# Optimization experiments

Hardware: AMD Instinct MI355X
Metric: run time of the kernel (lower is better)

## Reference

```python
import jax, jax.numpy as jnp
import numpy as np

N_X, N_UNITS, N_Y, N_U = 64, 256, 32, 64
BATCH = 32768


def setup_inputs() -> dict:
    key = jax.random.key(0)
    ks = jax.random.split(key, 10)
    nz = 2 * N_X + N_UNITS
    return {
        "u": jax.random.normal(ks[0], (BATCH, N_U, 1), dtype=jnp.float32),
        "x0": jax.random.normal(ks[1], (BATCH, N_X, 1), dtype=jnp.float32),
        # learned parameters (scaled down so H stays well-conditioned and tanh unsaturated)
        "B_2": 0.1 * jax.random.normal(ks[2], (N_X, N_U), dtype=jnp.float32),
        "C_2": 0.1 * jax.random.normal(ks[3], (N_Y, N_X), dtype=jnp.float32),
        "D_12": 0.1 * jax.random.normal(ks[4], (N_UNITS, N_U), dtype=jnp.float32),
        "D_21": 0.1 * jax.random.normal(ks[5], (N_Y, N_UNITS), dtype=jnp.float32),
        "b": 0.1 * jax.random.normal(ks[6], (N_X + N_UNITS + N_Y, 1), dtype=jnp.float32),
        "X": (1.0 / np.sqrt(nz)) * jax.random.normal(ks[7], (nz, nz), dtype=jnp.float32),
        "Y1": 0.1 * jax.random.normal(ks[8], (N_X, N_X), dtype=jnp.float32),
        # fixed IQC multipliers (train_qsr=False): Q nsd, R=I so Rinv=I; S stored transposed
        "S_t": 0.1 * jax.random.normal(ks[9], (N_U, N_Y), dtype=jnp.float32),
        "Q": -jnp.eye(N_Y, dtype=jnp.float32),
        "Rinv": jnp.eye(N_U, dtype=jnp.float32),
    }


def _constrained_weights(B_2, C_2, D_12, D_21, X, S_t, Q, Rinv):
    """Port of REN.updateConstrainedWeights (train_qsr=False). Returns C_1, D_11, lam."""
    n_x, n_units = B_2.shape[0], D_12.shape[0]
    n_y = C_2.shape[0]
    nz = 2 * n_x + n_units
    C2_ = S_t @ C_2                       # [n_u, n_x]
    D21_ = S_t @ D_21 - D_12.T            # [n_u, n_units]
    H = X.T @ X + 1e-3 * jnp.eye(nz, dtype=X.dtype)
    lT1 = jnp.concatenate([C2_.T, D21_.T, B_2], axis=0)          # [nz, n_u]
    H = H + lT1 @ Rinv @ lT1.T
    lT2 = jnp.concatenate([C_2.T, D_21.T, jnp.zeros((n_x, n_y), dtype=X.dtype)], axis=0)
    H = H - lT2 @ Q @ lT2.T
    H_21 = H[n_x:n_x + n_units, :n_x]
    H_22 = H[n_x:n_x + n_units, n_x:n_x + n_units]
    C_1 = -H_21                           # [n_units, n_x]
    lam = 0.5 * jnp.diag(H_22)            # Lambda diagonal, > 0 since H is PD
    # L = tril(-(H_22 - diag(H_22))) == -strictly_lower(H_22)
    D_11 = -jnp.tril(H_22, k=-1)          # strictly lower triangular [n_units, n_units]
    return C_1, D_11, lam


def _forward(u, x0, B_2, C_2, D_12, D_21, b, X, Y1, S_t, Q, Rinv):
    n_x, n_units = B_2.shape[0], D_12.shape[0]
    C_1, D_11, lam = _constrained_weights(B_2, C_2, D_12, D_21, X, S_t, Q, Rinv)
    u2 = u[:, :, 0]                       # [B, n_u]
    x2 = x0[:, :, 0]                      # [B, n_x]
    b_w = b[n_x:n_x + n_units, 0]         # [n_units]
    b_y = b[n_x + n_units:, 0]            # [n_y]
    # precompute the non-recurrent part of the pre-activation for all units
    v = x2 @ C_1.T + u2 @ D_12.T + b_w    # [B, n_units]
    # NOTE: the source uses D_11 row (i_unit - 1), not i_unit (faithful to original code).
    # For i=0 the source uses term2 = 0; D_11 is strictly lower so the full-row dot
    # against the partially-filled w (zeros beyond index i) matches D_11[i-1, :i] @ w[:i].
    Drows = jnp.concatenate([jnp.zeros((1, n_units), dtype=D_11.dtype), D_11[:-1]], axis=0)
    batch = u2.shape[0]

    def step(w, i):
        wi = jnp.tanh((v[:, i] + w @ Drows[i]) / lam[i])   # [B]
        w = w.at[:, i].set(wi)
        return w, None

    w0 = jnp.zeros((batch, n_units), dtype=v.dtype)
    w, _ = jax.lax.scan(step, w0, jnp.arange(n_units))
    y = x2 @ C_2.T + w @ D_21.T + b_y     # [B, n_y]
    return y[:, :, None]                  # [B, n_y, 1]


def reference(u, x0, B_2, C_2, D_12, D_21, b, X, Y1, S_t, Q, Rinv):
    return _forward(u, x0, B_2, C_2, D_12, D_21, b, X, Y1, S_t, Q, Rinv)
```

## Files before the change

kernel.cpp:

```cpp
#include <hip/hip_runtime.h>
#include <hip/hip_bf16.h>

typedef __attribute__((ext_vector_type(8))) short short8;
typedef __attribute__((ext_vector_type(4))) float floatx4;

__device__ inline unsigned short bf16_rn(float f) {
    return (unsigned short)((__float_as_uint(f) + 0x8000u) >> 16);
}
__device__ inline short8 pack8(float4 a, float4 b) {
    short8 r;
    r[0] = (short)bf16_rn(a.x); r[1] = (short)bf16_rn(a.y);
    r[2] = (short)bf16_rn(a.z); r[3] = (short)bf16_rn(a.w);
    r[4] = (short)bf16_rn(b.x); r[5] = (short)bf16_rn(b.y);
    r[6] = (short)bf16_rn(b.z); r[7] = (short)bf16_rn(b.w);
    return r;
}

__global__ __launch_bounds__(64) void ren_prep13(
    const float* __restrict__ B2, const float* __restrict__ C2,
    const float* __restrict__ D12, const float* __restrict__ D21,
    const float* __restrict__ St, const float* __restrict__ Q,
    const float* __restrict__ Rinv,
    float* __restrict__ lT1, float* __restrict__ t1,
    float* __restrict__ lT2, float* __restrict__ t2,
    unsigned short* __restrict__ Wvb, unsigned short* __restrict__ C2b,
    unsigned short* __restrict__ D21b)
{
    const int t = threadIdx.x;
    const int blk = blockIdx.x;
    if (blk >= 384) {
        const int id = (blk - 384) * 64 + t;
        if (id < 16384) {
            Wvb[(id >> 6) * 128 + 64 + (id & 63)] = bf16_rn(D12[id]);
        } else if (id < 16384 + 2048) {
            C2b[id - 16384] = bf16_rn(C2[id - 16384]);
        } else if (id < 16384 + 2048 + 8192) {
            D21b[id - 18432] = bf16_rn(D21[id - 18432]);
        }
        return;
    }

    __shared__ float stl[64 * 33];
    __shared__ float s1[64];
    __shared__ float s2[32];
#pragma unroll
    for (int j = 0; j < 32; j++) {
        const int id = j * 64 + t;
        stl[(id >> 5) * 33 + (id & 31)] = St[id];
    }
    __syncthreads();

    const int r = blk;
    const int c = t;

    float v1;
    if (r < 64) {
        float s = 0.f;
#pragma unroll
        for (int p = 0; p < 32; p++) s += stl[c * 33 + p] * C2[p * 64 + r];
        v1 = s;
    } else if (r < 320) {
        const int j = r - 64;
        float s = 0.f;
#pragma unroll
        for (int p = 0; p < 32; p++) s += stl[c * 33 + p] * D21[p * 256 + j];
        v1 = s - D12[j * 64 + c];
    } else {
        v1 = B2[(r - 320) * 64 + c];
    }
    s1[c] = v1;
    lT1[r * 64 + c] = v1;

    if (c < 32) {
        float v2;
        if (r < 64)       v2 = C2[c * 64 + r];
        else if (r < 320) v2 = D21[c * 256 + (r - 64)];
        else              v2 = 0.f;
        s2[c] = v2;
        lT2[r * 32 + c] = v2;
    }
    __syncthreads();

    float a = 0.f;
#pragma unroll
    for (int k = 0; k < 64; k++) a += s1[k] * Rinv[k * 64 + c];
    t1[r * 64 + c] = a;

    if (c < 32) {
        float bq = 0.f;
#pragma unroll
        for (int k = 0; k < 32; k++) bq += s2[k] * Q[k * 32 + c];
        t2[r * 32 + c] = bq;
    }
}

__global__ __launch_bounds__(320) void ren_prep2(
    const float* __restrict__ X,
    const float* __restrict__ lT1, const float* __restrict__ t1,
    const float* __restrict__ lT2, const float* __restrict__ t2,
    unsigned short* __restrict__ Wvb, unsigned short* __restrict__ Drowsb,
    float* __restrict__ Dtri, float* __restrict__ laminv)
{
    const int c = threadIdx.x;
    const int i = blockIdx.x;
    const float* __restrict__ xr = X + 64 + i;

    float f0 = 0.f, f1 = 0.f, f2 = 0.f, f3 = 0.f;
    for (int k0 = 0; k0 < 384; k0 += 8) {
        float xc[8], xu[8];
#pragma unroll
        for (int kk = 0; kk < 8; kk++) {
            xc[kk] = X[(k0 + kk) * 384 + c];
            xu[kk] = xr[(k0 + kk) * 384];
        }
        f0 += xu[0] * xc[0]; f1 += xu[1] * xc[1];
        f2 += xu[2] * xc[2]; f3 += xu[3] * xc[3];
        f0 += xu[4] * xc[4]; f1 += xu[5] * xc[5];
        f2 += xu[6] * xc[6]; f3 += xu[7] * xc[7];
    }

    const float* __restrict__ t1r = t1 + (64 + i) * 64;
    const float* __restrict__ l1r = lT1 + c * 64;
#pragma unroll
    for (int m4 = 0; m4 < 16; m4++) {
        const float4 lv = *(const float4*)(l1r + m4 * 4);
        f0 += t1r[m4 * 4 + 0] * lv.x; f1 += t1r[m4 * 4 + 1] * lv.y;
        f2 += t1r[m4 * 4 + 2] * lv.z; f3 += t1r[m4 * 4 + 3] * lv.w;
    }
    const float* __restrict__ t2r = t2 + (64 + i) * 32;
    const float* __restrict__ l2r = lT2 + c * 32;
#pragma unroll
    for (int m4 = 0; m4 < 8; m4++) {
        const float4 lv = *(const float4*)(l2r + m4 * 4);
        f0 -= t2r[m4 * 4 + 0] * lv.x; f1 -= t2r[m4 * 4 + 1] * lv.y;
        f2 -= t2r[m4 * 4 + 2] * lv.z; f3 -= t2r[m4 * 4 + 3] * lv.w;
    }
    float acc = (f0 + f1) + (f2 + f3) + (((64 + i) == c) ? 0.001f : 0.f);

    if (c < 64) {
        Wvb[i * 128 + c] = bf16_rn(-acc);
    } else {
        const int cb = c - 64;
        if (cb == i) laminv[i] = 2.0f / acc;
        if (i < 255) {
            const float dv = (cb <= i - 1) ? -acc : 0.f;
            Drowsb[(i + 1) * 256 + cb] = bf16_rn(dv);
            if (((i + 1) >> 4) == (cb >> 4))
                Dtri[((i + 1) >> 4) * 256 + ((i + 1) & 15) * 16 + (cb & 15)] = dv;
        } else {
            Drowsb[cb] = 0;
        }
    }
}

__global__ __launch_bounds__(64) void ren_main(
    const float* __restrict__ u, const float* __restrict__ x0,
    const float* __restrict__ b,
    const unsigned short* __restrict__ Wvb,
    const unsigned short* __restrict__ Drowsb,
    const float* __restrict__ Dtri,
    const float* __restrict__ laminv,
    const unsigned short* __restrict__ C2b,
    const unsigned short* __restrict__ D21b,
    float* __restrict__ out)
{
    __shared__ float buf[16][20];

    const int L = threadIdx.x;
    const int col = L & 15;
    const int quad = L >> 4;
    const int row0 = blockIdx.x * 16;

    short8 zf[4];
#pragma unroll
    for (int c = 0; c < 4; c++) {
        const float* p = (c < 2 ? x0 : u) + (row0 + col) * 64 + (c & 1) * 32 + quad * 8;
        const float4 lo = *(const float4*)p;
        const float4 hi = *(const float4*)(p + 4);
        zf[c] = pack8(lo, hi);
    }

    const short8 zero8 = {0, 0, 0, 0, 0, 0, 0, 0};
    short8 wf[8];
#pragma unroll
    for (int c = 0; c < 8; c++) wf[c] = zero8;

    short8 vf[2][4], hf[2][8];
#pragma unroll
    for (int c = 0; c < 4; c++)
        vf[0][c] = *(const short8*)(Wvb + col * 128 + c * 32 + quad * 8);
#pragma unroll
    for (int c = 0; c < 8; c++) { hf[0][c] = zero8; hf[1][c] = zero8; }

#pragma unroll
    for (int n = 0; n < 16; n++) {
        const int cur = n & 1, nxt = cur ^ 1;

        if (n < 15) {
#pragma unroll
            for (int c = 0; c < 4; c++)
                vf[nxt][c] = *(const short8*)(Wvb + (16 * (n + 1) + col) * 128 + c * 32 + quad * 8);
#pragma unroll
            for (int c = 0; c < 8; c++)
                if (c < ((n + 2) >> 1))
                    hf[nxt][c] = *(const short8*)(Drowsb + (16 * (n + 1) + col) * 256 + c * 32 + quad * 8);
        }

        floatx4 acc = {0.f, 0.f, 0.f, 0.f};
#pragma unroll
        for (int c = 0; c < 4; c++)
            acc = __builtin_amdgcn_mfma_f32_16x16x32_bf16(zf[c], vf[cur][c], acc, 0, 0, 0);
#pragma unroll
        for (int c = 0; c < 8; c++)
            if (c < ((n + 1) >> 1))
                acc = __builtin_amdgcn_mfma_f32_16x16x32_bf16(wf[c], hf[cur][c], acc, 0, 0, 0);

        const float bw = b[64 + 16 * n + col];
#pragma unroll
        for (int r = 0; r < 4; r++)
            buf[quad * 4 + r][col] = acc[r] + bw;

        if (L < 16) {
            float vl[16];
#pragma unroll
            for (int p4 = 0; p4 < 4; p4++) {
                const float4 tv = *(const float4*)&buf[L][p4 * 4];
                vl[p4 * 4 + 0] = tv.x; vl[p4 * 4 + 1] = tv.y;
                vl[p4 * 4 + 2] = tv.z; vl[p4 * 4 + 3] = tv.w;
            }
            float wl[16];
#pragma unroll
            for (int q = 0; q < 16; q++) {
                float aa = vl[q], ab = 0.f;
                const float* __restrict__ dq = Dtri + n * 256 + q * 16;
#pragma unroll
                for (int p = 0; p + 2 <= q; p++) {
                    const float d = dq[p];
                    if (p & 1) ab += d * wl[p];
                    else       aa += d * wl[p];
                }
                float a = (aa + ab) * laminv[16 * n + q];
                a = fminf(15.f, fmaxf(-15.f, a));
                const float e = __expf(2.f * a);
                wl[q] = (e - 1.f) * __builtin_amdgcn_rcpf(e + 1.f);
            }
#pragma unroll
            for (int p4 = 0; p4 < 4; p4++)
                *(float4*)&buf[L][p4 * 4] = make_float4(
                    wl[p4 * 4], wl[p4 * 4 + 1], wl[p4 * 4 + 2], wl[p4 * 4 + 3]);
        }

        {
            const float4 wlo = *(const float4*)&buf[col][(quad & 1) * 8];
            const float4 whi = *(const float4*)&buf[col][(quad & 1) * 8 + 4];
            const short8 nf = pack8(wlo, whi);
            const int cc = n >> 1;
            if ((n & 1) == 0) {
                wf[cc] = (quad < 2) ? nf : zero8;
            } else {
                if (quad >= 2) wf[cc] = nf;
            }
        }
    }

    floatx4 yacc0 = {0.f, 0.f, 0.f, 0.f};
    floatx4 yacc1 = {0.f, 0.f, 0.f, 0.f};
#pragma unroll
    for (int c = 0; c < 2; c++) {
        const short8 b0 = *(const short8*)(C2b + col * 64 + c * 32 + quad * 8);
        const short8 b1 = *(const short8*)(C2b + (16 + col) * 64 + c * 32 + quad * 8);
        yacc0 = __builtin_amdgcn_mfma_f32_16x16x32_bf16(zf[c], b0, yacc0, 0, 0, 0);
        yacc1 = __builtin_amdgcn_mfma_f32_16x16x32_bf16(zf[c], b1, yacc1, 0, 0, 0);
    }
#pragma unroll
    for (int c = 0; c < 8; c++) {
        const short8 b0 = *(const short8*)(D21b + col * 256 + c * 32 + quad * 8);
        const short8 b1 = *(const short8*)(D21b + (16 + col) * 256 + c * 32 + quad * 8);
        yacc0 = __builtin_amdgcn_mfma_f32_16x16x32_bf16(wf[c], b0, yacc0, 0, 0, 0);
        yacc1 = __builtin_amdgcn_mfma_f32_16x16x32_bf16(wf[c], b1, yacc1, 0, 0, 0);
    }
    const float by0 = b[320 + col];
    const float by1 = b[320 + 16 + col];
#pragma unroll
    for (int r = 0; r < 4; r++) {
        out[(row0 + quad * 4 + r) * 32 + col]      = yacc0[r] + by0;
        out[(row0 + quad * 4 + r) * 32 + 16 + col] = yacc1[r] + by1;
    }
}

extern "C" void kernel_launch(void* const* d_in, const int* in_sizes, int n_in,
                              void* d_out, int out_size, void* d_ws, size_t ws_size,
                              hipStream_t stream)
{
    const float* u    = (const float*)d_in[0];
    const float* x0   = (const float*)d_in[1];
    const float* B2   = (const float*)d_in[2];
    const float* C2   = (const float*)d_in[3];
    const float* D12  = (const float*)d_in[4];
    const float* D21  = (const float*)d_in[5];
    const float* b    = (const float*)d_in[6];
    const float* X    = (const float*)d_in[7];
    const float* St   = (const float*)d_in[9];
    const float* Q    = (const float*)d_in[10];
    const float* Rinv = (const float*)d_in[11];
    float* out = (float*)d_out;

    float* ws     = (float*)d_ws;
    float* lT1    = ws;
    float* t1     = lT1 + 384 * 64;
    float* lT2    = t1 + 384 * 64;
    float* t2     = lT2 + 384 * 32;
    float* laminv = t2 + 384 * 32;
    float* Dtri   = laminv + 256;
    unsigned short* Drowsb = (unsigned short*)(Dtri + 16 * 256);
    unsigned short* Wvb    = Drowsb + 256 * 256;
    unsigned short* C2b    = Wvb + 256 * 128;
    unsigned short* D21b   = C2b + 32 * 64;

    ren_prep13<<<dim3(800), dim3(64), 0, stream>>>(B2, C2, D12, D21, St, Q, Rinv,
                                                   lT1, t1, lT2, t2, Wvb, C2b, D21b);
    ren_prep2<<<dim3(256), dim3(320), 0, stream>>>(X, lT1, t1, lT2, t2,
                                                   Wvb, Drowsb, Dtri, laminv);

    const int batch = in_sizes[0] / 64;
    ren_main<<<dim3(batch / 16), dim3(64), 0, stream>>>(u, x0, b, Wvb, Drowsb,
                                                        Dtri, laminv, C2b, D21b, out);
}
```

Measured before the change: 153.1 us.

## Stage per-block constants in LDS, run tanh on all lanes, pipeline prep loads

In the main kernel, the per-block triangular D block, lambda scales and biases are staged into LDS. The tanh recurrence now runs redundantly on all 64 lanes instead of 16, which removes the write-back to shared memory and the readback. Tanh uses exp2 with log2e folded into the lambda scale, and MFMA accumulation is split across two chains. C2 fragments are prefetched in the last iteration. The prep kernels cache the X column and the C2/D21 column in LDS and software-pipeline the X loads. The redundant per-lane serial tanh work and extra LDS traffic may offset the gains.

```diff
diff --git a/kernel.cpp b/kernel.cpp
--- a/kernel.cpp
+++ b/kernel.cpp
@@ -4,15 +4,15 @@
 typedef __attribute__((ext_vector_type(8))) short short8;
 typedef __attribute__((ext_vector_type(4))) float floatx4;
 
+#define MFMA16 __builtin_amdgcn_mfma_f32_16x16x32_bf16
+
 __device__ inline unsigned short bf16_rn(float f) {
     return (unsigned short)((__float_as_uint(f) + 0x8000u) >> 16);
 }
-__device__ inline short8 pack8(float4 a, float4 b) {
+__device__ inline short8 pack8(const float* v) {
     short8 r;
-    r[0] = (short)bf16_rn(a.x); r[1] = (short)bf16_rn(a.y);
-    r[2] = (short)bf16_rn(a.z); r[3] = (short)bf16_rn(a.w);
-    r[4] = (short)bf16_rn(b.x); r[5] = (short)bf16_rn(b.y);
-    r[6] = (short)bf16_rn(b.z); r[7] = (short)bf16_rn(b.w);
+#pragma unroll
+    for (int j = 0; j < 8; j++) r[j] = (short)bf16_rn(v[j]);
     return r;
 }
 
@@ -41,42 +41,39 @@
     }
 
     __shared__ float stl[64 * 33];
+    __shared__ float colbuf[32];
     __shared__ float s1[64];
-    __shared__ float s2[32];
+
+    const int r = blk;
+    const int c = t;
 #pragma unroll
     for (int j = 0; j < 32; j++) {
         const int id = j * 64 + t;
         stl[(id >> 5) * 33 + (id & 31)] = St[id];
     }
+    if (t < 32)
+        colbuf[t] = (r < 64) ? C2[t * 64 + r]
+                  : (r < 320 ? D21[t * 256 + (r - 64)] : 0.f);
     __syncthreads();
-
-    const int r = blk;
-    const int c = t;
 
     float v1;
     if (r < 64) {
         float s = 0.f;
 #pragma unroll
-        for (int p = 0; p < 32; p++) s += stl[c * 33 + p] * C2[p * 64 + r];
+        for (int p = 0; p < 32; p++) s += stl[c * 33 + p] * colbuf[p];
         v1 = s;
     } else if (r < 320) {
-        const int j = r - 64;
         float s = 0.f;
 #pragma unroll
-        for (int p = 0; p < 32; p++) s += stl[c * 33 + p] * D21[p * 256 + j];
-        v1 = s - D12[j * 64 + c];
+        for (int p = 0; p < 32; p++) s += stl[c * 33 + p] * colbuf[p];
+        v1 = s - D12[(r - 64) * 64 + c];
     } else {
         v1 = B2[(r - 320) * 64 + c];
     }
     s1[c] = v1;
     lT1[r * 64 + c] = v1;
-
     if (c < 32) {
-        float v2;
-        if (r < 64)       v2 = C2[c * 64 + r];
-        else if (r < 320) v2 = D21[c * 256 + (r - 64)];
-        else              v2 = 0.f;
-        s2[c] = v2;
+        const float v2 = (r < 320) ? colbuf[c] : 0.f;
         lT2[r * 32 + c] = v2;
     }
     __syncthreads();
@@ -89,7 +86,7 @@
     if (c < 32) {
         float bq = 0.f;
 #pragma unroll
-        for (int k = 0; k < 32; k++) bq += s2[k] * Q[k * 32 + c];
+        for (int k = 0; k < 32; k++) bq += colbuf[k] * Q[k * 32 + c];
         t2[r * 32 + c] = bq;
     }
 }
@@ -99,24 +96,37 @@
     const float* __restrict__ lT1, const float* __restrict__ t1,
     const float* __restrict__ lT2, const float* __restrict__ t2,
     unsigned short* __restrict__ Wvb, unsigned short* __restrict__ Drowsb,
-    float* __restrict__ Dtri, float* __restrict__ laminv)
+    float* __restrict__ Dtri, float* __restrict__ lamg)
 {
+    __shared__ float xcol[384];
     const int c = threadIdx.x;
     const int i = blockIdx.x;
-    const float* __restrict__ xr = X + 64 + i;
+    for (int t = c; t < 384; t += 320) xcol[t] = X[t * 384 + 64 + i];
+    __syncthreads();
 
     float f0 = 0.f, f1 = 0.f, f2 = 0.f, f3 = 0.f;
-    for (int k0 = 0; k0 < 384; k0 += 8) {
-        float xc[8], xu[8];
+    float ac[8], au[8], bc8[8], bu[8];
+#pragma unroll
+    for (int kk = 0; kk < 8; kk++) { ac[kk] = X[kk * 384 + c]; au[kk] = xcol[kk]; }
+    for (int k0 = 0; k0 < 384; k0 += 16) {
 #pragma unroll
         for (int kk = 0; kk < 8; kk++) {
-            xc[kk] = X[(k0 + kk) * 384 + c];
-            xu[kk] = xr[(k0 + kk) * 384];
-        }
-        f0 += xu[0] * xc[0]; f1 += xu[1] * xc[1];
-        f2 += xu[2] * xc[2]; f3 += xu[3] * xc[3];
-        f0 += xu[4] * xc[4]; f1 += xu[5] * xc[5];
-        f2 += xu[6] * xc[6]; f3 += xu[7] * xc[7];
+            bc8[kk] = X[(k0 + 8 + kk) * 384 + c]; bu[kk] = xcol[k0 + 8 + kk];
+        }
+        f0 += au[0] * ac[0]; f1 += au[1] * ac[1];
+        f2 += au[2] * ac[2]; f3 += au[3] * ac[3];
+        f0 += au[4] * ac[4]; f1 += au[5] * ac[5];
+        f2 += au[6] * ac[6]; f3 += au[7] * ac[7];
+        if (k0 + 16 < 384) {
+#pragma unroll
+            for (int kk = 0; kk < 8; kk++) {
+                ac[kk] = X[(k0 + 16 + kk) * 384 + c]; au[kk] = xcol[k0 + 16 + kk];
+            }
+        }
+        f0 += bu[0] * bc8[0]; f1 += bu[1] * bc8[1];
+        f2 += bu[2] * bc8[2]; f3 += bu[3] * bc8[3];
+        f0 += bu[4] * bc8[4]; f1 += bu[5] * bc8[5];
+        f2 += bu[6] * bc8[6]; f3 += bu[7] * bc8[7];
     }
 
     const float* __restrict__ t1r = t1 + (64 + i) * 64;
@@ -141,7 +151,8 @@
         Wvb[i * 128 + c] = bf16_rn(-acc);
     } else {
         const int cb = c - 64;
-        if (cb == i) laminv[i] = 2.0f / acc;
+        if (i == 0 && cb < 16) Dtri[cb] = 0.f;
+        if (cb == i) lamg[i] = 5.7707801635558536f / acc;
         if (i < 255) {
             const float dv = (cb <= i - 1) ? -acc : 0.f;
             Drowsb[(i + 1) * 256 + cb] = bf16_rn(dv);
@@ -159,25 +170,35 @@
     const unsigned short* __restrict__ Wvb,
     const unsigned short* __restrict__ Drowsb,
     const float* __restrict__ Dtri,
-    const float* __restrict__ laminv,
+    const float* __restrict__ lamg,
     const unsigned short* __restrict__ C2b,
     const unsigned short* __restrict__ D21b,
     float* __restrict__ out)
 {
     __shared__ float buf[16][20];
+    __shared__ float dblk[256];
+    __shared__ float lamsh[256];
+    __shared__ float bsh[256];
 
     const int L = threadIdx.x;
     const int col = L & 15;
     const int quad = L >> 4;
     const int row0 = blockIdx.x * 16;
 
+#pragma unroll
+    for (int j = 0; j < 4; j++) {
+        lamsh[j * 64 + L] = lamg[j * 64 + L];
+        bsh[j * 64 + L]   = b[64 + j * 64 + L];
+    }
+
     short8 zf[4];
 #pragma unroll
     for (int c = 0; c < 4; c++) {
-        const float* p = (c < 2 ? x0 : u) + (row0 + col) * 64 + (c & 1) * 32 + quad * 8;
-        const float4 lo = *(const float4*)p;
-        const float4 hi = *(const float4*)(p + 4);
-        zf[c] = pack8(lo, hi);
+        const float* p = (c < 2 ? x0 : u) + (long)(row0 + col) * 64 + (c & 1) * 32 + quad * 8;
+        float t[8];
+        *(float4*)&t[0] = *(const float4*)p;
+        *(float4*)&t[4] = *(const float4*)(p + 4);
+        zf[c] = pack8(t);
     }
 
     const short8 zero8 = {0, 0, 0, 0, 0, 0, 0, 0};
@@ -185,7 +206,8 @@
 #pragma unroll
     for (int c = 0; c < 8; c++) wf[c] = zero8;
 
-    short8 vf[2][4], hf[2][8];
+    short8 vf[2][4], hf[2][8], yc[4];
+    float4 dt = *(const float4*)(Dtri + 4 * L);
 #pragma unroll
     for (int c = 0; c < 4; c++)
         vf[0][c] = *(const short8*)(Wvb + col * 128 + c * 32 + quad * 8);
@@ -196,7 +218,10 @@
     for (int n = 0; n < 16; n++) {
         const int cur = n & 1, nxt = cur ^ 1;
 
+        *(float4*)&dblk[4 * L] = dt;
+
         if (n < 15) {
+            dt = *(const float4*)(Dtri + (n + 1) * 256 + 4 * L);
 #pragma unroll
             for (int c = 0; c < 4; c++)
                 vf[nxt][c] = *(const short8*)(Wvb + (16 * (n + 1) + col) * 128 + c * 32 + quad * 8);
@@ -204,87 +229,84 @@
             for (int c = 0; c < 8; c++)
                 if (c < ((n + 2) >> 1))
                     hf[nxt][c] = *(const short8*)(Drowsb + (16 * (n + 1) + col) * 256 + c * 32 + quad * 8);
-        }
-
-        floatx4 acc = {0.f, 0.f, 0.f, 0.f};
-#pragma unroll
-        for (int c = 0; c < 4; c++)
-            acc = __builtin_amdgcn_mfma_f32_16x16x32_bf16(zf[c], vf[cur][c], acc, 0, 0, 0);
+        } else {
+            yc[0] = *(const short8*)(C2b + col * 64 + quad * 8);
+            yc[1] = *(const short8*)(C2b + col * 64 + 32 + quad * 8);
+            yc[2] = *(const short8*)(C2b + (16 + col) * 64 + quad * 8);
+            yc[3] = *(const short8*)(C2b + (16 + col) * 64 + 32 + quad * 8);
+        }
+
+        floatx4 acc0 = {0.f, 0.f, 0.f, 0.f}, acc1 = {0.f, 0.f, 0.f, 0.f};
+        acc0 = MFMA16(zf[0], vf[cur][0], acc0, 0, 0, 0);
+        acc1 = MFMA16(zf[1], vf[cur][1], acc1, 0, 0, 0);
+        acc0 = MFMA16(zf[2], vf[cur][2], acc0, 0, 0, 0);
+        acc1 = MFMA16(zf[3], vf[cur][3], acc1, 0, 0, 0);
 #pragma unroll
         for (int c = 0; c < 8; c++)
-            if (c < ((n + 1) >> 1))
-                acc = __builtin_amdgcn_mfma_f32_16x16x32_bf16(wf[c], hf[cur][c], acc, 0, 0, 0);
-
-        const float bw = b[64 + 16 * n + col];
+            if (c < ((n + 1) >> 1)) {
+                if (c & 1) acc1 = MFMA16(wf[c], hf[cur][c], acc1, 0, 0, 0);
+                else       acc0 = MFMA16(wf[c], hf[cur][c], acc0, 0, 0, 0);
+            }
+
+        const float bwv = bsh[16 * n + col];
 #pragma unroll
         for (int r = 0; r < 4; r++)
-            buf[quad * 4 + r][col] = acc[r] + bw;
-
-        if (L < 16) {
-            float vl[16];
-#pragma unroll
-            for (int p4 = 0; p4 < 4; p4++) {
-                const float4 tv = *(const float4*)&buf[L][p4 * 4];
-                vl[p4 * 4 + 0] = tv.x; vl[p4 * 4 + 1] = tv.y;
-                vl[p4 * 4 + 2] = tv.z; vl[p4 * 4 + 3] = tv.w;
+            buf[quad * 4 + r][col] = acc0[r] + acc1[r] + bwv;
+
+        float vl[16], lmv[16];
+#pragma unroll
+        for (int p4 = 0; p4 < 4; p4++) {
+            *(float4*)&vl[p4 * 4]  = *(const float4*)&buf[col][p4 * 4];
+            *(float4*)&lmv[p4 * 4] = *(const float4*)&lamsh[16 * n + p4 * 4];
+        }
+
+        float wl[16];
+#pragma unroll
+        for (int q = 0; q < 16; q++) wl[q] = 0.f;
+#pragma unroll
+        for (int q = 0; q < 16; q++) {
+            float aa = vl[q], ab = 0.f;
+            const int nb = (q >= 2) ? ((q + 2) >> 2) : 0;
+#pragma unroll
+            for (int p4 = 0; p4 < nb; p4++) {
+                const float4 d4 = *(const float4*)&dblk[q * 16 + p4 * 4];
+                aa += d4.x * wl[p4 * 4 + 0];
+                ab += d4.y * wl[p4 * 4 + 1];
+                aa += d4.z * wl[p4 * 4 + 2];
+                ab += d4.w * wl[p4 * 4 + 3];
             }
-            float wl[16];
-#pragma unroll
-            for (int q = 0; q < 16; q++) {
-                float aa = vl[q], ab = 0.f;
-                const float* __restrict__ dq = Dtri + n * 256 + q * 16;
-#pragma unroll
-                for (int p = 0; p + 2 <= q; p++) {
-                    const float d = dq[p];
-                    if (p & 1) ab += d * wl[p];
-                    else       aa += d * wl[p];
-                }
-                float a = (aa + ab) * laminv[16 * n + q];
-                a = fminf(15.f, fmaxf(-15.f, a));
-                const float e = __expf(2.f * a);
-                wl[q] = (e - 1.f) * __builtin_amdgcn_rcpf(e + 1.f);
-            }
-#pragma unroll
-            for (int p4 = 0; p4 < 4; p4++)
-                *(float4*)&buf[L][p4 * 4] = make_float4(
-                    wl[p4 * 4], wl[p4 * 4 + 1], wl[p4 * 4 + 2], wl[p4 * 4 + 3]);
+            float tt = (aa + ab) * lmv[q];
+            tt = fminf(44.f, fmaxf(-44.f, tt));
+            const float e = __builtin_amdgcn_exp2f(tt);
+            wl[q] = 1.f - 2.f * __builtin_amdgcn_rcpf(e + 1.f);
         }
 
         {
-            const float4 wlo = *(const float4*)&buf[col][(quad & 1) * 8];
-            const float4 whi = *(const float4*)&buf[col][(quad & 1) * 8 + 4];
-            const short8 nf = pack8(wlo, whi);
+            const short8 nf = pack8(&wl[(quad & 1) * 8]);
             const int cc = n >> 1;
-            if ((n & 1) == 0) {
-                wf[cc] = (quad < 2) ? nf : zero8;
-            } else {
-                if (quad >= 2) wf[cc] = nf;
-            }
-        }
-    }
-
-    floatx4 yacc0 = {0.f, 0.f, 0.f, 0.f};
-    floatx4 yacc1 = {0.f, 0.f, 0.f, 0.f};
-#pragma unroll
-    for (int c = 0; c < 2; c++) {
-        const short8 b0 = *(const short8*)(C2b + col * 64 + c * 32 + quad * 8);
-        const short8 b1 = *(const short8*)(C2b + (16 + col) * 64 + c * 32 + quad * 8);
-        yacc0 = __builtin_amdgcn_mfma_f32_16x16x32_bf16(zf[c], b0, yacc0, 0, 0, 0);
-        yacc1 = __builtin_amdgcn_mfma_f32_16x16x32_bf16(zf[c], b1, yacc1, 0, 0, 0);
-    }
+            if ((n & 1) == 0) wf[cc] = (quad < 2) ? nf : zero8;
+            else if (quad >= 2) wf[cc] = nf;
+        }
+    }
+
+    floatx4 y0 = {0.f, 0.f, 0.f, 0.f}, y1 = {0.f, 0.f, 0.f, 0.f};
+    y0 = MFMA16(zf[0], yc[0], y0, 0, 0, 0);
+    y1 = MFMA16(zf[0], yc[2], y1, 0, 0, 0);
+    y0 = MFMA16(zf[1], yc[1], y0, 0, 0, 0);
+    y1 = MFMA16(zf[1], yc[3], y1, 0, 0, 0);
 #pragma unroll
     for (int c = 0; c < 8; c++) {
         const short8 b0 = *(const short8*)(D21b + col * 256 + c * 32 + quad * 8);
         const short8 b1 = *(const short8*)(D21b + (16 + col) * 256 + c * 32 + quad * 8);
-        yacc0 = __builtin_amdgcn_mfma_f32_16x16x32_bf16(wf[c], b0, yacc0, 0, 0, 0);
-        yacc1 = __builtin_amdgcn_mfma_f32_16x16x32_bf16(wf[c], b1, yacc1, 0, 0, 0);
+        y0 = MFMA16(wf[c], b0, y0, 0, 0, 0);
+        y1 = MFMA16(wf[c], b1, y1, 0, 0, 0);
     }
     const float by0 = b[320 + col];
-    const float by1 = b[320 + 16 + col];
+    const float by1 = b[336 + col];
 #pragma unroll
     for (int r = 0; r < 4; r++) {
-        out[(row0 + quad * 4 + r) * 32 + col]      = yacc0[r] + by0;
-        out[(row0 + quad * 4 + r) * 32 + 16 + col] = yacc1[r] + by1;
+        out[(long)(row0 + quad * 4 + r) * 32 + col]      = y0[r] + by0;
+        out[(long)(row0 + quad * 4 + r) * 32 + 16 + col] = y1[r] + by1;
     }
 }
 
@@ -310,8 +332,8 @@
     float* t1     = lT1 + 384 * 64;
     float* lT2    = t1 + 384 * 64;
     float* t2     = lT2 + 384 * 32;
-    float* laminv = t2 + 384 * 32;
-    float* Dtri   = laminv + 256;
+    float* lamg   = t2 + 384 * 32;
+    float* Dtri   = lamg + 256;
     unsigned short* Drowsb = (unsigned short*)(Dtri + 16 * 256);
     unsigned short* Wvb    = Drowsb + 256 * 256;
     unsigned short* C2b    = Wvb + 256 * 128;
@@ -320,9 +342,9 @@
     ren_prep13<<<dim3(800), dim3(64), 0, stream>>>(B2, C2, D12, D21, St, Q, Rinv,
                                                    lT1, t1, lT2, t2, Wvb, C2b, D21b);
     ren_prep2<<<dim3(256), dim3(320), 0, stream>>>(X, lT1, t1, lT2, t2,
-                                                   Wvb, Drowsb, Dtri, laminv);
+                                                   Wvb, Drowsb, Dtri, lamg);
 
     const int batch = in_sizes[0] / 64;
     ren_main<<<dim3(batch / 16), dim3(64), 0, stream>>>(u, x0, b, Wvb, Drowsb,
-                                                        Dtri, laminv, C2b, D21b, out);
-}
+                                                        Dtri, lamg, C2b, D21b, out);
+}
```

Result: faster. 146.3 us (-4.4%).
